# Kernel tuning notes

Hardware: AMD Instinct MI355X
Metric: run time of the kernel (lower is better)

The kernel has to match this reference:

```python
import jax, jax.numpy as jnp
import numpy as np
import math

B, S, D, H = 4, 2048, 2048, 16
HD = D // H  # 128


def _alibi_slopes(n_heads):
    # standard ALiBi slopes: 2^(-8/n * (h+1))
    return jnp.asarray([2.0 ** (-8.0 / n_heads * (h + 1)) for h in range(n_heads)], dtype=jnp.float32)


def setup_inputs() -> dict:
    key = jax.random.key(0)
    ks = jax.random.split(key, 10)
    w = lambda k: jax.random.normal(k, (D, D), dtype=jnp.float32) * 0.02
    b = lambda k: jax.random.normal(k, (D,), dtype=jnp.float32) * 0.01
    return {
        "hidden_states": jax.random.normal(ks[0], (B, S, D), dtype=jnp.float32),
        "Wq": w(ks[1]), "bq": b(ks[2]),
        "Wk": w(ks[3]), "bk": b(ks[4]),
        "Wv": w(ks[5]), "bv": b(ks[6]),
        "Wo": w(ks[7]), "bo": b(ks[8]),
        "alibi_slopes": _alibi_slopes(H),
    }


def reference(hidden_states, Wq, bq, Wk, bk, Wv, bv, Wo, bo, alibi_slopes):
    Bn, t, _ = hidden_states.shape
    split = lambda x: x.reshape(Bn, t, H, HD).transpose(0, 2, 1, 3)  # [B,H,S,hd]
    q = split(hidden_states @ Wq.T + bq)
    k = split(hidden_states @ Wk.T + bk)
    v = split(hidden_states @ Wv.T + bv)

    scores = jnp.einsum("bhsd,bhtd->bhst", q, k)  # [B,H,S,S]
    pos = jnp.arange(t)
    # alibi bias added BEFORE the 1/sqrt(hd) scaling, as in the torch code
    rel = (pos[None, :] - pos[:, None]).astype(scores.dtype)  # j - i
    bias = alibi_slopes[:, None, None] * rel  # [H,S,S]
    scores = (scores + bias[None]) / math.sqrt(HD)
    # grok-style tanh rescaling
    scores = 30.0 * jnp.tanh(scores / 30.0)
    causal = pos[:, None] >= pos[None, :]  # [S,S]
    scores = jnp.where(causal[None, None], scores, -jnp.inf)
    probs = jax.nn.softmax(scores, axis=-1)
    ctx = jnp.einsum("bhst,bhtd->bhsd", probs, v)
    ctx = ctx.transpose(0, 2, 1, 3).reshape(Bn, t, D)
    return ctx @ Wo.T + bo
```

## Files before the change

### kernel.cpp

```cpp
#include <hip/hip_runtime.h>

typedef unsigned int u32;
typedef unsigned short u16;
typedef __bf16 bf16x8 __attribute__((ext_vector_type(8)));
typedef float f32x4 __attribute__((ext_vector_type(4)));


__device__ __forceinline__ u16 f2bf(float f) {
  u32 u = __builtin_bit_cast(u32, f);
  u32 r = u + 0x7fffu + ((u >> 16) & 1u);
  return (u16)(r >> 16);
}

__device__ __forceinline__ void gload_lds16(const void* g, void* l) {
  __builtin_amdgcn_global_load_lds(
      (__attribute__((address_space(1))) void*)(g),
      (__attribute__((address_space(3))) void*)(l), 16, 0, 0);
}


__global__ __launch_bounds__(256) void convert_kernel(
    const float* __restrict__ hs, const float* __restrict__ wq,
    const float* __restrict__ wk, const float* __restrict__ wv,
    const float* __restrict__ wo,
    u16* __restrict__ hsb, u16* __restrict__ wqb, u16* __restrict__ wkb,
    u16* __restrict__ wvb, u16* __restrict__ wob) {
  long t = (long)blockIdx.x * 256 + threadIdx.x;
  const float* src;
  u16* dst;
  long off;
  if (t < 2097152) {
    src = hs; dst = hsb; off = t << 3;
  } else {
    long u = t - 2097152;
    int wi = (int)(u >> 19);
    off = (u & 524287) << 3;
    if (wi == 0)      { src = wq; dst = wqb; }
    else if (wi == 1) { src = wk; dst = wkb; }
    else if (wi == 2) { src = wv; dst = wvb; }
    else              { src = wo; dst = wob; }
  }
  float4 a = *(const float4*)(src + off);
  float4 b = *(const float4*)(src + off + 4);
  uint4 o;
  o.x = (u32)f2bf(a.x) | ((u32)f2bf(a.y) << 16);
  o.y = (u32)f2bf(a.z) | ((u32)f2bf(a.w) << 16);
  o.z = (u32)f2bf(b.x) | ((u32)f2bf(b.y) << 16);
  o.w = (u32)f2bf(b.z) | ((u32)f2bf(b.w) << 16);
  *(uint4*)(dst + off) = o;
}


template <int OF32>
__global__ __launch_bounds__(512, 2) void gemm256_kernel(
    const u16* __restrict__ A, const u16* __restrict__ Bw,
    const float* __restrict__ bias0, const float* __restrict__ bias1,
    const float* __restrict__ bias2, void* __restrict__ o0,
    void* __restrict__ o1, void* __restrict__ o2, int m_tiles, int n_tiles) {
  __shared__ __align__(16) char L[2][2][2][16384];

  const int tid = threadIdx.x;
  const int lane = tid & 63, w = tid >> 6;
  const int lr = lane & 15, lk = lane >> 4;
  const int wm = (w >> 2) * 128, wn = (w & 3) * 64;

  const int bid = blockIdx.x;
  const int xcd = bid & 7, loc = bid >> 3;
  const int n_idx = xcd * (n_tiles >> 3) + loc / m_tiles;
  const int m_idx = loc % m_tiles;
  const int m0 = m_idx * 256, n0 = n_idx * 256;

  const char* Ab = (const char*)A;
  const char* Bb = (const char*)Bw;
  const char* gA[2];
  const char* gB[2];
#pragma unroll
  for (int j = 0; j < 2; j++) {
    const int o = j * 8192 + tid * 16;
    const int row = o >> 6;
    const int c = (o & 63) ^ (((row >> 1) & 3) << 4);
    gA[j] = Ab + (size_t)(m0 + row) * 4096 + c;
    gB[j] = Bb + (size_t)(n0 + row) * 4096 + c;
  }

  auto stage = [&](int t, int kh, int isB) {
    char* Ld = &L[t & 1][isB][kh][0] + tid * 16;
    const int gof = t * 128 + kh * 64;
#pragma unroll
    for (int j = 0; j < 2; j++)
      gload_lds16((isB ? gB[j] : gA[j]) + gof, Ld + j * 8192);
  };
  auto rdA = [&](bf16x8* dst, int buf, int kh, int mset) {
#pragma unroll
    for (int m = 0; m < 4; m++) {
      const int row = wm + mset * 64 + m * 16 + lr;
      const int c = (lk * 16) ^ (((row >> 1) & 3) << 4);
      dst[m] = *(const bf16x8*)(&L[buf][0][kh][0] + row * 64 + c);
    }
  };
  auto rdB = [&](bf16x8* dst, int buf, int kh) {
#pragma unroll
    for (int n = 0; n < 4; n++) {
      const int row = wn + n * 16 + lr;
      const int c = (lk * 16) ^ (((row >> 1) & 3) << 4);
      dst[n] = *(const bf16x8*)(&L[buf][1][kh][0] + row * 64 + c);
    }
  };

  f32x4 acc[2][4][4];
#pragma unroll
  for (int s = 0; s < 2; s++)
#pragma unroll
    for (int m = 0; m < 4; m++)
#pragma unroll
      for (int n = 0; n < 4; n++) acc[s][m][n] = {0.f, 0.f, 0.f, 0.f};

  auto mm = [&](f32x4 (&ac)[4][4], bf16x8* a_, bf16x8* b_) {
    __builtin_amdgcn_s_setprio(1);
#pragma unroll
    for (int m = 0; m < 4; m++)
#pragma unroll
      for (int n = 0; n < 4; n++)
        ac[m][n] = __builtin_amdgcn_mfma_f32_16x16x32_bf16(a_[m], b_[n],
                                                           ac[m][n], 0, 0, 0);
    __builtin_amdgcn_s_setprio(0);
  };

  stage(0, 0, 0); stage(0, 0, 1); stage(0, 1, 0); stage(0, 1, 1);

  bf16x8 aP[4], aQ[4], b0[4], b1[4];
  for (int t = 0; t < 32; ++t) {
    const int buf = t & 1;
    const int t1 = (t + 1 < 32) ? t + 1 : 31;
    asm volatile("s_waitcnt vmcnt(4)" ::: "memory");
    asm volatile("s_barrier" ::: "memory");
    rdA(aP, buf, 0, 0);
    rdB(b0, buf, 0);
    stage(t1, 0, 0);
    if (t) mm(acc[1], aQ, b1);
    rdA(aQ, buf, 0, 1);
    stage(t1, 0, 1);
    mm(acc[0], aP, b0);
    asm volatile("s_waitcnt vmcnt(4)" ::: "memory");
    asm volatile("s_barrier" ::: "memory");
    rdA(aP, buf, 1, 0);
    rdB(b1, buf, 1);
    stage(t1, 1, 0);
    mm(acc[1], aQ, b0);
    rdA(aQ, buf, 1, 1);
    stage(t1, 1, 1);
    mm(acc[0], aP, b1);
  }
  mm(acc[1], aQ, b1);

  const float* bias;
  void* op;
  int nl0;
  if (OF32) {
    bias = bias0; op = o0; nl0 = n0;
  } else {
    const int seg = n0 >> 11;
    bias = seg == 0 ? bias0 : (seg == 1 ? bias1 : bias2);
    op = seg == 0 ? o0 : (seg == 1 ? o1 : o2);
    nl0 = n0 & 2047;
  }
#pragma unroll
  for (int n = 0; n < 4; n++) {
    const int col = nl0 + wn + n * 16 + lr;
    const float bv = bias[col];
#pragma unroll
    for (int s = 0; s < 2; s++)
#pragma unroll
      for (int m = 0; m < 4; m++) {
        const int grow = m0 + wm + s * 64 + m * 16 + lk * 4;
#pragma unroll
        for (int r = 0; r < 4; r++) {
          const float v = acc[s][m][n][r] + bv;
          if (OF32)
            ((float*)op)[(size_t)(grow + r) * 2048 + col] = v;
          else
            ((u16*)op)[(size_t)(grow + r) * 2048 + col] = f2bf(v);
        }
      }
  }
}


__global__ __launch_bounds__(512, 2) void attn_kernel(
    const u16* __restrict__ Qm, const u16* __restrict__ Km,
    const u16* __restrict__ Vm, const float* __restrict__ slopes,
    u16* __restrict__ ctx) {
  __shared__ __align__(16) char Ks[64 * 256];
  __shared__ __align__(16) char Vt[2][128 * 128];
  __shared__ __align__(16) char Pb[8][16 * 128];

  const int bid = blockIdx.x;
  const int sw = (bid & 7) * 64 + (bid >> 3);
  const int bh = sw >> 3, pi = sw & 7;
  const int b = bh >> 4, h = bh & 15;
  const int NTA = 2 * pi + 2;

  const int tid = threadIdx.x;
  const int lane = tid & 63, w = tid >> 6;
  const int lr = lane & 15, lk = lane >> 4;

  const char* Qb = (const char*)Qm + (size_t)b * 2048 * 4096 + h * 256;
  const char* Kb = (const char*)Km + (size_t)b * 2048 * 4096 + h * 256;
  const char* Vb = (const char*)Vm + (size_t)b * 2048 * 4096 + h * 256;

  const float SCALE = 0.08838834764831845f;
  const float sl_c = slopes[h] * SCALE;

  const float A0 = 1363.3468136400704f, A2 = 0.16831442143704573f,
              A4 = 1.7811049887518067e-6f;
  const float D0 = 945.0f, D2 = 0.4666666666666667f, D4 = 1.851851851851852e-5f;
  const float SH = -43.2808512266689f;

  float Tt[16];
#pragma unroll
  for (int nb = 0; nb < 4; nb++)
#pragma unroll
    for (int r = 0; r < 4; r++) Tt[nb * 4 + r] = sl_c * (float)(nb * 16 - r);

  const int vd0 = (tid & 15) * 8;
  const int vkv2 = tid >> 4;

  uint4 vr0, vr1;

  auto kvt_of = [&](int it) { return it < NTA ? it : it - NTA; };

  auto stageK = [&](int it) {
    const int kv0 = kvt_of(it) * 64;
#pragma unroll
    for (int j = 0; j < 2; j++) {
      const int o = j * 8192 + tid * 16;
      const int row = o >> 8, c = (o & 255) ^ ((row & 7) << 4);
      gload_lds16(Kb + (size_t)(kv0 + row) * 4096 + c, Ks + o);
    }
  };
  auto loadV = [&](int it) {
    const int kv0 = kvt_of(it) * 64;
    vr0 = *(const uint4*)(Vb + (size_t)(kv0 + vkv2 * 2) * 4096 + vd0 * 2);
    vr1 = *(const uint4*)(Vb + (size_t)(kv0 + vkv2 * 2 + 1) * 4096 + vd0 * 2);
  };
  auto writeV = [&](int bufi) {
    const u32* p0 = (const u32*)&vr0;
    const u32* p1 = (const u32*)&vr1;
#pragma unroll
    for (int wd = 0; wd < 4; wd++) {
      const u32 ev = __builtin_amdgcn_perm(p1[wd], p0[wd], 0x05040100u);
      const u32 od = __builtin_amdgcn_perm(p1[wd], p0[wd], 0x07060302u);
      const int d0_ = vd0 + 2 * wd, d1_ = d0_ + 1;
      *(u32*)(Vt[bufi] + d0_ * 128 +
              ((vkv2 * 4) ^ (((d0_ ^ (d0_ >> 3)) & 7) << 4))) = ev;
      *(u32*)(Vt[bufi] + d1_ * 128 +
              ((vkv2 * 4) ^ (((d1_ ^ (d1_ >> 3)) & 7) << 4))) = od;
    }
  };

  bf16x8 qf[4];
  f32x4 pv[8];
  float rs[4];
  int q0 = 0;

  stageK(0);
  loadV(0);

  for (int it = 0; it < 34; ++it) {
    const int bufi = it & 1;
    const int kv0 = kvt_of(it) * 64;

    if (it == 0 || it == NTA) {
      const int st = (it == 0) ? pi : (15 - pi);
      q0 = st * 128 + w * 16;
#pragma unroll
      for (int kc = 0; kc < 4; kc++)
        qf[kc] =
            *(const bf16x8*)(Qb + (size_t)(q0 + lr) * 4096 + kc * 64 + lk * 16);
#pragma unroll
      for (int i = 0; i < 8; i++) pv[i] = {0.f, 0.f, 0.f, 0.f};
      rs[0] = rs[1] = rs[2] = rs[3] = 0.f;
    }

    writeV(bufi);
    asm volatile("s_waitcnt vmcnt(0)" ::: "memory");
    __syncthreads();

    if (it + 1 < 34) loadV(it + 1);

    f32x4 sc[4];
    __builtin_amdgcn_s_setprio(1);
#pragma unroll
    for (int nb = 0; nb < 4; nb++) {
      f32x4 a = {0.f, 0.f, 0.f, 0.f};
      const int krow = nb * 16 + lr;
#pragma unroll
      for (int kc = 0; kc < 4; kc++) {
        const int off = krow * 256 + ((kc * 64 + lk * 16) ^ ((krow & 7) << 4));
        bf16x8 kf = *(const bf16x8*)(Ks + off);
        a = __builtin_amdgcn_mfma_f32_16x16x32_bf16(qf[kc], kf, a, 0, 0, 0);
      }
      sc[nb] = a;
    }
    __builtin_amdgcn_s_setprio(0);

    __syncthreads();
    if (it + 1 < 34) stageK(it + 1);

    const float aliB = sl_c * (float)(kv0 + lr - q0 - lk * 4);
#pragma unroll
    for (int nb = 0; nb < 4; nb++) {
      const int kv = kv0 + nb * 16 + lr;
#pragma unroll
      for (int r = 0; r < 4; r++) {
        const int q = q0 + lk * 4 + r;
        const float z = fmaf(sc[nb][r], SCALE, aliB + Tt[nb * 4 + r]);
        const float u = z * z;
        const float num = fmaf(u, fmaf(u, A4, A2), A0);
        const float den = fmaf(u, fmaf(u, D4, D2), D0);
        const float pa = fmaf(z * num, __builtin_amdgcn_rcpf(den), SH);
        float p = exp2f(pa);
        p = (kv <= q) ? p : 0.0f;
        rs[r] += p;
        const int qq = lk * 4 + r;
        const int off =
            qq * 128 + (((nb * 16 + lr) * 2) ^ ((qq & 12) << 3));
        const u32 ub = __builtin_bit_cast(u32, p);
        *(u16*)(Pb[w] + off) = (u16)((ub + 0x8000u) >> 16);
      }
    }

    __builtin_amdgcn_s_setprio(1);
#pragma unroll
    for (int kc = 0; kc < 2; kc++) {
      const int poff = lr * 128 + ((kc * 64 + lk * 16) ^ ((lr & 12) << 3));
      bf16x8 pf = *(const bf16x8*)(Pb[w] + poff);
#pragma unroll
      for (int db = 0; db < 8; db++) {
        const int d = db * 16 + lr;
        const int voff =
            d * 128 + ((kc * 64 + lk * 16) ^ (((d ^ (d >> 3)) & 7) << 4));
        bf16x8 vf = *(const bf16x8*)(Vt[bufi] + voff);
        pv[db] = __builtin_amdgcn_mfma_f32_16x16x32_bf16(pf, vf, pv[db], 0, 0, 0);
      }
    }
    __builtin_amdgcn_s_setprio(0);

    if (it == NTA - 1 || it == 33) {
      float inv[4];
#pragma unroll
      for (int r = 0; r < 4; r++) {
        float s = rs[r];
        s += __shfl_xor(s, 1);
        s += __shfl_xor(s, 2);
        s += __shfl_xor(s, 4);
        s += __shfl_xor(s, 8);
        inv[r] = 1.0f / s;
      }
      const size_t baserow = (size_t)b * 2048 + q0 + lk * 4;
#pragma unroll
      for (int db = 0; db < 8; db++)
#pragma unroll
        for (int r = 0; r < 4; r++)
          ctx[(baserow + r) * 2048 + h * 128 + db * 16 + lr] =
              f2bf(pv[db][r] * inv[r]);
    }
  }
}


extern "C" void kernel_launch(void* const* d_in, const int* in_sizes, int n_in,
                              void* d_out, int out_size, void* d_ws,
                              size_t ws_size, hipStream_t stream) {
  const float* hs = (const float*)d_in[0];
  const float* Wq = (const float*)d_in[1];
  const float* bq = (const float*)d_in[2];
  const float* Wk = (const float*)d_in[3];
  const float* bk = (const float*)d_in[4];
  const float* Wv = (const float*)d_in[5];
  const float* bv = (const float*)d_in[6];
  const float* Wo = (const float*)d_in[7];
  const float* bo = (const float*)d_in[8];
  const float* slopes = (const float*)d_in[9];

  char* ws = (char*)d_ws;
  u16* hsb = (u16*)(ws);
  u16* wqb = (u16*)(ws + 33554432);
  u16* wkb = (u16*)(ws + 41943040);
  u16* wvb = (u16*)(ws + 50331648);
  u16* wob = (u16*)(ws + 58720256);
  u16* Qb  = (u16*)(ws + 67108864);
  u16* Kb  = (u16*)(ws + 100663296);
  u16* Vb  = (u16*)(ws + 134217728);
  u16* ctxb = hsb;

  convert_kernel<<<16384, 256, 0, stream>>>(hs, Wq, Wk, Wv, Wo, hsb, wqb, wkb,
                                            wvb, wob);
  gemm256_kernel<0><<<768, 512, 0, stream>>>(hsb, wqb, bq, bk, bv, Qb, Kb, Vb,
                                             32, 24);
  attn_kernel<<<512, 512, 0, stream>>>(Qb, Kb, Vb, slopes, ctxb);
  gemm256_kernel<1><<<256, 512, 0, stream>>>(ctxb, wob, bo, bo, bo, d_out,
                                             d_out, d_out, 32, 8);
}
```

Baseline: 509.5 us.

## Restructure GEMM main loop into barrier-separated MFMA clusters with A-prefetch two ahead

```diff
diff --git a/kernel.cpp b/kernel.cpp
--- a/kernel.cpp
+++ b/kernel.cpp
@@ -17,6 +17,13 @@
       (__attribute__((address_space(1))) void*)(g),
       (__attribute__((address_space(3))) void*)(l), 16, 0, 0);
 }
+
+#define BARRIER asm volatile("s_barrier" ::: "memory")
+#define LGKM0                                         \
+  do {                                                \
+    asm volatile("s_waitcnt lgkmcnt(0)" ::: "memory"); \
+    __builtin_amdgcn_sched_barrier(0);                \
+  } while (0)
 
 
 __global__ __launch_bounds__(256) void convert_kernel(
@@ -90,21 +97,25 @@
     for (int j = 0; j < 2; j++)
       gload_lds16((isB ? gB[j] : gA[j]) + gof, Ld + j * 8192);
   };
-  auto rdA = [&](bf16x8* dst, int buf, int kh, int mset) {
-#pragma unroll
-    for (int m = 0; m < 4; m++) {
-      const int row = wm + mset * 64 + m * 16 + lr;
-      const int c = (lk * 16) ^ (((row >> 1) & 3) << 4);
-      dst[m] = *(const bf16x8*)(&L[buf][0][kh][0] + row * 64 + c);
-    }
-  };
-  auto rdB = [&](bf16x8* dst, int buf, int kh) {
-#pragma unroll
-    for (int n = 0; n < 4; n++) {
-      const int row = wn + n * 16 + lr;
-      const int c = (lk * 16) ^ (((row >> 1) & 3) << 4);
-      dst[n] = *(const bf16x8*)(&L[buf][1][kh][0] + row * 64 + c);
-    }
+  auto rdA8 = [&](bf16x8* dst, int buf, int s) {
+#pragma unroll
+    for (int kh = 0; kh < 2; kh++)
+#pragma unroll
+      for (int mf = 0; mf < 4; mf++) {
+        const int row = wm + s * 64 + mf * 16 + lr;
+        const int c = (lk * 16) ^ (((row >> 1) & 3) << 4);
+        dst[kh * 4 + mf] = *(const bf16x8*)(&L[buf][0][kh][0] + row * 64 + c);
+      }
+  };
+  auto rdB4 = [&](bf16x8* dst, int buf, int nh) {
+#pragma unroll
+    for (int kh = 0; kh < 2; kh++)
+#pragma unroll
+      for (int nf = 0; nf < 2; nf++) {
+        const int row = wn + nh * 32 + nf * 16 + lr;
+        const int c = (lk * 16) ^ (((row >> 1) & 3) << 4);
+        dst[kh * 2 + nf] = *(const bf16x8*)(&L[buf][1][kh][0] + row * 64 + c);
+      }
   };
 
   f32x4 acc[2][4][4];
@@ -115,43 +126,52 @@
 #pragma unroll
       for (int n = 0; n < 4; n++) acc[s][m][n] = {0.f, 0.f, 0.f, 0.f};
 
-  auto mm = [&](f32x4 (&ac)[4][4], bf16x8* a_, bf16x8* b_) {
+  auto clus = [&](int s, int nh, bf16x8* A8, bf16x8* B4) {
     __builtin_amdgcn_s_setprio(1);
 #pragma unroll
-    for (int m = 0; m < 4; m++)
-#pragma unroll
-      for (int n = 0; n < 4; n++)
-        ac[m][n] = __builtin_amdgcn_mfma_f32_16x16x32_bf16(a_[m], b_[n],
-                                                           ac[m][n], 0, 0, 0);
+    for (int kh = 0; kh < 2; kh++)
+#pragma unroll
+      for (int mf = 0; mf < 4; mf++)
+#pragma unroll
+        for (int nf = 0; nf < 2; nf++)
+          acc[s][mf][nh * 2 + nf] = __builtin_amdgcn_mfma_f32_16x16x32_bf16(
+              A8[kh * 4 + mf], B4[kh * 2 + nf], acc[s][mf][nh * 2 + nf], 0, 0, 0);
     __builtin_amdgcn_s_setprio(0);
   };
 
-  stage(0, 0, 0); stage(0, 0, 1); stage(0, 1, 0); stage(0, 1, 1);
-
-  bf16x8 aP[4], aQ[4], b0[4], b1[4];
+  stage(0, 0, 0); stage(0, 1, 0); stage(0, 0, 1); stage(0, 1, 1);
+  stage(1, 0, 0); stage(1, 1, 0);
+  asm volatile("s_waitcnt vmcnt(4)" ::: "memory");
+  BARRIER;
+
+  bf16x8 A8[8], B0f[4], B1f[4];
   for (int t = 0; t < 32; ++t) {
     const int buf = t & 1;
-    const int t1 = (t + 1 < 32) ? t + 1 : 31;
+    const int tB = (t + 1 < 32) ? t + 1 : 31;
+    const int tA = (t + 2 < 32) ? t + 2 : 31;
+    rdA8(A8, buf, 0);
+    rdB4(B0f, buf, 0);
+    stage(tB, 0, 1);
+    BARRIER; LGKM0;
+    clus(0, 0, A8, B0f);
+    BARRIER;
+    rdB4(B1f, buf, 1);
+    stage(tB, 1, 1);
+    BARRIER; LGKM0;
+    clus(0, 1, A8, B1f);
+    BARRIER;
+    rdA8(A8, buf, 1);
+    BARRIER; LGKM0;
+    clus(1, 0, A8, B0f);
+    BARRIER;
+    stage(tA, 0, 0);
+    stage(tA, 1, 0);
+    BARRIER; LGKM0;
+    clus(1, 1, A8, B1f);
     asm volatile("s_waitcnt vmcnt(4)" ::: "memory");
-    asm volatile("s_barrier" ::: "memory");
-    rdA(aP, buf, 0, 0);
-    rdB(b0, buf, 0);
-    stage(t1, 0, 0);
-    if (t) mm(acc[1], aQ, b1);
-    rdA(aQ, buf, 0, 1);
-    stage(t1, 0, 1);
-    mm(acc[0], aP, b0);
-    asm volatile("s_waitcnt vmcnt(4)" ::: "memory");
-    asm volatile("s_barrier" ::: "memory");
-    rdA(aP, buf, 1, 0);
-    rdB(b1, buf, 1);
-    stage(t1, 1, 0);
-    mm(acc[1], aQ, b0);
-    rdA(aQ, buf, 1, 1);
-    stage(t1, 1, 1);
-    mm(acc[0], aP, b1);
-  }
-  mm(acc[1], aQ, b1);
+    BARRIER;
+  }
+  asm volatile("s_waitcnt vmcnt(0)" ::: "memory");
 
   const float* bias;
   void* op;
```

Measured after the change: 481.8 us. 1.06x faster.
